# Kernel tuning notes

Measured on AMD Instinct MI355X. Metric: run time of the kernel, lower is better.

## Reference

```python
import jax, jax.numpy as jnp
import numpy as np

N_NODES = 50000   # n_nodes (adjacency is [N,N])
NNZ = 800000      # nonzeros per support (avg degree 16)
S = 3             # number of supports
D_IN = 512
D_OUT = 256


def setup_inputs() -> dict:
    key = jax.random.key(0)
    k0, k1, k2, k3, k4, k5 = jax.random.split(key, 6)
    x = jax.random.normal(k0, (N_NODES, D_IN), dtype=jnp.float32)
    # glorot-uniform per-support weights, stacked [S, D_IN, D_OUT]
    scale = float(np.sqrt(6.0 / (D_IN + D_OUT)))
    W = jax.random.uniform(k1, (S, D_IN, D_OUT), dtype=jnp.float32, minval=-scale, maxval=scale)
    rows = jax.random.randint(k2, (S, NNZ), 0, N_NODES, dtype=jnp.int32)
    cols = jax.random.randint(k3, (S, NNZ), 0, N_NODES, dtype=jnp.int32)
    vals = jax.random.uniform(k4, (S, NNZ), dtype=jnp.float32)
    # Conv1d(in=S, out=1, k=1, bias=False) == learned weighted sum over supports
    cw = jax.random.normal(k5, (S,), dtype=jnp.float32) * 0.5
    return {"x": x, "W": W, "rows": rows, "cols": cols, "vals": vals, "cw": cw}


def reference(x, W, rows, cols, vals, cw):
    # mod='output': out = relu( sum_i cw[i] * (A_i @ (x @ W_i)) )
    def spmm(r, c, v, pre):
        # A in COO: out[r] += v * pre[c]
        msgs = v[:, None] * pre[c]          # [NNZ, D_OUT] gather
        return jax.ops.segment_sum(msgs, r, num_segments=N_NODES)

    out = jnp.zeros((N_NODES, D_OUT), dtype=x.dtype)
    for i in range(S):                      # small fixed support count
        pre = x @ W[i]                      # dense GEMM [N, D_OUT]
        out = out + cw[i] * spmm(rows[i], cols[i], vals[i], pre)
    return jax.nn.relu(out)
```

## Files before the change

### kernel.cpp

```cpp
#include <hip/hip_runtime.h>
#include <stdint.h>

#define N_NODES 50000
#define N_PAD   50048
#define NNZ     800000
#define SUP     3
#define D_IN    512
#define D_OUT   256
#define TOT_E   (SUP * NNZ)
#define NBUCK   782
#define CAP     3680
#define CHUNK   3072
#define NBB     782
#define NB_WPREP 1536
#define NB_XPREP 12500
#define NB_GEMM  2346

typedef __attribute__((ext_vector_type(8))) short bf16x8;
typedef __attribute__((ext_vector_type(4))) float f32x4;
typedef __attribute__((address_space(3))) unsigned int lds_u32_t;
typedef const __attribute__((address_space(1))) unsigned int glb_u32_t;

static __device__ __forceinline__ unsigned short f2bf(float f) {
    unsigned int u = __float_as_uint(f);
    unsigned int r = (u + 0x7fffu + ((u >> 16) & 1u)) >> 16;
    return (unsigned short)r;
}
static __device__ __forceinline__ unsigned int pack_bf2(float lo, float hi) {
    unsigned int a = __float_as_uint(lo) + 0x8000u;
    unsigned int b = __float_as_uint(hi) + 0x8000u;
    return (a >> 16) | (b & 0xffff0000u);
}
static __device__ __forceinline__ float bf2f(unsigned short h) {
    return __uint_as_float(((unsigned int)h) << 16);
}
static __device__ __forceinline__ int2 ldnt_int2(const int2* p) {
    long long v = __builtin_nontemporal_load((const long long*)p);
    int2 r;
    r.x = (int)(v & 0xffffffffLL);
    r.y = (int)(v >> 32);
    return r;
}

__global__ __launch_bounds__(256) void prepbucket_kernel(const int* __restrict__ rows,
                                                         const int* __restrict__ cols,
                                                         const float* __restrict__ vals,
                                                         const float* __restrict__ cw,
                                                         int* __restrict__ bucket_cursor,
                                                         int2* __restrict__ buck,
                                                         const float* __restrict__ x,
                                                         unsigned int* __restrict__ xb,
                                                         const float* __restrict__ W,
                                                         unsigned short* __restrict__ Wt) {
    __shared__ double smem8[5536];
    char* smem = (char*)smem8;
    const int blk = blockIdx.x;
    const int tid = threadIdx.x;

    if (blk < NBB) {
        int2* stage = (int2*)smem;
        unsigned short* bucket_of = (unsigned short*)(smem + 24576);
        int* hist   = (int*)(smem + 30720);
        int* sc     = (int*)(smem + 33848);
        int* sstart = (int*)(smem + 34872);
        int* lcur   = (int*)(smem + 38000);
        int* gbase  = (int*)(smem + 41128);

        const int base_n = blk * CHUNK;
        const int count = min(CHUNK, TOT_E - base_n);
        float cw0 = cw[0], cw1 = cw[1], cw2 = cw[2];

        for (int i = tid; i < NBUCK; i += 256) hist[i] = 0;
        __syncthreads();
        for (int i = tid; i < count; i += 256)
            atomicAdd(&hist[rows[base_n + i] >> 6], 1);
        __syncthreads();
        const int lo = tid * 4;
        const int hi = min(lo + 4, NBUCK);
        int acc = 0;
        for (int i = lo; i < hi; ++i) acc += hist[i];
        sc[tid] = acc;
        __syncthreads();
        for (int off = 1; off < 256; off <<= 1) {
            int t = (tid >= off) ? sc[tid - off] : 0;
            __syncthreads();
            sc[tid] += t;
            __syncthreads();
        }
        int run = sc[tid] - acc;
        for (int i = lo; i < hi; ++i) {
            int h = hist[i];
            sstart[i] = run;
            lcur[i]   = run;
            run += h;
        }
        __syncthreads();
        for (int i = tid; i < NBUCK; i += 256)
            gbase[i] = atomicAdd(&bucket_cursor[i], hist[i]);
        __syncthreads();
        for (int i = tid; i < count; i += 256) {
            int n = base_n + i;
            int r = rows[n];
            int c = __builtin_nontemporal_load(&cols[n]);
            float v = __builtin_nontemporal_load(&vals[n]);
            int s = n / NNZ;
            float w = v * (s == 0 ? cw0 : (s == 1 ? cw1 : cw2));
            int b = r >> 6;
            int p = atomicAdd(&lcur[b], 1);
            stage[p] = make_int2(((r & 63) << 18) | (s * N_NODES + c), __float_as_int(w));
            bucket_of[p] = (unsigned short)b;
        }
        __syncthreads();
        for (int i = tid; i < count; i += 256) {
            int b = bucket_of[i];
            int local_off = i - sstart[b];
            buck[(size_t)b * CAP + gbase[b] + local_off] = stage[i];
        }
    } else if (blk < NBB + NB_XPREP) {
        int idx = (blk - NBB) * 256 + tid;
        const f32x4* src = (const f32x4*)(x) + idx * 2;
        f32x4 f0 = __builtin_nontemporal_load(src);
        f32x4 f1 = __builtin_nontemporal_load(src + 1);
        uint4 o;
        o.x = pack_bf2(f0.x, f0.y);
        o.y = pack_bf2(f0.z, f0.w);
        o.z = pack_bf2(f1.x, f1.y);
        o.w = pack_bf2(f1.z, f1.w);
        *((uint4*)xb + idx) = o;
    } else {
        int idx = (blk - NBB - NB_XPREP) * 256 + tid;
        int n = idx & (D_OUT - 1);
        int k = (idx >> 8) & (D_IN - 1);
        int s = idx >> 17;
        Wt[((size_t)s * D_OUT + n) * D_IN + k] = f2bf(W[idx]);
    }
}

__global__ __launch_bounds__(256) void sortgemm_kernel(const int2* __restrict__ buck,
                                                       const int* __restrict__ bucket_cursor,
                                                       int2* __restrict__ cv,
                                                       int* __restrict__ base,
                                                       int* __restrict__ cnt,
                                                       const unsigned short* __restrict__ xb,
                                                       const unsigned short* __restrict__ Wt,
                                                       unsigned short* __restrict__ pre) {
    __shared__ double smem8[4096];
    char* smem = (char*)smem8;
    const int blk = blockIdx.x;
    const int tid = threadIdx.x;

    if (blk < NBUCK) {
        int2* stage = (int2*)smem;
        int* hist   = (int*)(smem + 29440);
        int* sc     = (int*)(smem + 29696);
        int* sstart = (int*)(smem + 29952);
        int* cur    = (int*)(smem + 30208);

        const int b = blk;
        const int sz = bucket_cursor[b];
        const int2* src = buck + (size_t)b * CAP;

        if (tid < 64) hist[tid] = 0;
        __syncthreads();
        for (int i = tid; i < sz; i += 256)
            atomicAdd(&hist[((unsigned)src[i].x) >> 18], 1);
        __syncthreads();
        if (tid < 64) sc[tid] = hist[tid];
        __syncthreads();
        for (int off = 1; off < 64; off <<= 1) {
            int t = (tid >= off && tid < 64) ? sc[tid - off] : 0;
            __syncthreads();
            if (tid < 64) sc[tid] += t;
            __syncthreads();
        }
        if (tid < 64) {
            int st = sc[tid] - hist[tid];
            sstart[tid] = st;
            cur[tid] = st;
        }
        __syncthreads();
        for (int i = tid; i < sz; i += 256) {
            int2 e = src[i];
            int rl = ((unsigned)e.x) >> 18;
            int p = atomicAdd(&cur[rl], 1);
            stage[p] = make_int2(e.x & 0x3FFFF, e.y);
        }
        __syncthreads();
        size_t gb = (size_t)b * CAP;
        for (int i = tid; i < sz; i += 256) cv[gb + i] = stage[i];
        int r = b * 64 + tid;
        if (tid < 64 && r < N_NODES) {
            base[r] = (int)gb + sstart[tid];
            cnt[r]  = hist[tid];
        }
    } else {
        unsigned short* lds_a = (unsigned short*)smem;
        unsigned short* lds_b = (unsigned short*)(smem + 16384);
        const int gblk = blk - NBUCK;
        constexpr int SWQ = NB_GEMM / 8;
        constexpr int SWR = NB_GEMM % 8;
        const int xcd = gblk & 7, pos = gblk >> 3;
        const int my = (xcd < SWR ? xcd * (SWQ + 1)
                                  : SWR * (SWQ + 1) + (xcd - SWR) * SWQ) + pos;
        const int mt  = my / 6;
        const int rem = my % 6;
        const int m0 = mt * 128;
        const int n0 = (rem & 1) * 128;
        const int s  = rem >> 1;
        const unsigned short* wt = Wt + (size_t)s * D_OUT * D_IN;
        const int wave = tid >> 6;
        const int lane = tid & 63;
        const int quad = lane >> 4;
        const int lo   = lane & 15;
        const int wm = (wave & 1) * 64;
        const int wn = (wave >> 1) * 64;

        f32x4 acc[4][4] = {};

        for (int kb = 0; kb < D_IN; kb += 64) {
            __syncthreads();
            #pragma unroll
            for (int c = 0; c < 4; ++c) {
                int idx = c * 256 + tid;
                int row = idx >> 3;
                int kp  = idx & 7;
                const unsigned short* ga = xb + (size_t)(m0 + row) * D_IN + kb + kp * 8;
                __builtin_amdgcn_global_load_lds((glb_u32_t*)ga,
                                                 (lds_u32_t*)&lds_a[idx * 8], 16, 0, 0);
                const unsigned short* gb = wt + (size_t)(n0 + row) * D_IN + kb + kp * 8;
                __builtin_amdgcn_global_load_lds((glb_u32_t*)gb,
                                                 (lds_u32_t*)&lds_b[idx * 8], 16, 0, 0);
            }
            __syncthreads();

            #pragma unroll
            for (int t = 0; t < 2; ++t) {
                bf16x8 af[4], bfr[4];
                #pragma unroll
                for (int i = 0; i < 4; ++i)
                    af[i] = *(const bf16x8*)&lds_a[(wm + 16 * i + lo) * 64 + t * 32 + quad * 8];
                #pragma unroll
                for (int j = 0; j < 4; ++j)
                    bfr[j] = *(const bf16x8*)&lds_b[(wn + 16 * j + lo) * 64 + t * 32 + quad * 8];
                #pragma unroll
                for (int i = 0; i < 4; ++i)
                    #pragma unroll
                    for (int j = 0; j < 4; ++j)
                        acc[i][j] = __builtin_amdgcn_mfma_f32_16x16x32_bf16(af[i], bfr[j], acc[i][j], 0, 0, 0);
            }
        }

        #pragma unroll
        for (int i = 0; i < 4; ++i) {
            #pragma unroll
            for (int j = 0; j < 4; ++j) {
                int gn = n0 + wn + 16 * j + lo;
                #pragma unroll
                for (int r = 0; r < 4; ++r) {
                    int gm2 = m0 + wm + 16 * i + quad * 4 + r;
                    if (gm2 < N_NODES)
                        pre[((size_t)s * N_NODES + gm2) * D_OUT + gn] = f2bf(acc[i][j][r]);
                }
            }
        }
    }
}

__global__ __launch_bounds__(256) void spmm_kernel(const unsigned short* __restrict__ pre,
                                                   const int* __restrict__ base,
                                                   const int* __restrict__ cnt,
                                                   const int2* __restrict__ cv,
                                                   float* __restrict__ out) {
    int row  = blockIdx.x * 4 + (threadIdx.x >> 6);
    int lane = threadIdx.x & 63;
    int start = base[row];
    int end   = start + cnt[row];
    float a0 = 0.f, a1 = 0.f, a2 = 0.f, a3 = 0.f;
    int j = start;
    for (; j + 16 <= end; j += 16) {
        int2 e[16];
        #pragma unroll
        for (int q = 0; q < 16; ++q) e[q] = ldnt_int2(&cv[j + q]);
        ushort4 p[16];
        #pragma unroll
        for (int q = 0; q < 16; ++q)
            p[q] = *(const ushort4*)(pre + (size_t)e[q].x * D_OUT + lane * 4);
        #pragma unroll
        for (int q = 0; q < 16; ++q) {
            float w = __int_as_float(e[q].y);
            a0 += w * bf2f(p[q].x);
            a1 += w * bf2f(p[q].y);
            a2 += w * bf2f(p[q].z);
            a3 += w * bf2f(p[q].w);
        }
    }
    for (; j + 8 <= end; j += 8) {
        int2 e[8];
        #pragma unroll
        for (int q = 0; q < 8; ++q) e[q] = ldnt_int2(&cv[j + q]);
        ushort4 p[8];
        #pragma unroll
        for (int q = 0; q < 8; ++q)
            p[q] = *(const ushort4*)(pre + (size_t)e[q].x * D_OUT + lane * 4);
        #pragma unroll
        for (int q = 0; q < 8; ++q) {
            float w = __int_as_float(e[q].y);
            a0 += w * bf2f(p[q].x);
            a1 += w * bf2f(p[q].y);
            a2 += w * bf2f(p[q].z);
            a3 += w * bf2f(p[q].w);
        }
    }
    for (; j + 4 <= end; j += 4) {
        int2 e[4];
        #pragma unroll
        for (int q = 0; q < 4; ++q) e[q] = ldnt_int2(&cv[j + q]);
        ushort4 p[4];
        #pragma unroll
        for (int q = 0; q < 4; ++q)
            p[q] = *(const ushort4*)(pre + (size_t)e[q].x * D_OUT + lane * 4);
        #pragma unroll
        for (int q = 0; q < 4; ++q) {
            float w = __int_as_float(e[q].y);
            a0 += w * bf2f(p[q].x);
            a1 += w * bf2f(p[q].y);
            a2 += w * bf2f(p[q].z);
            a3 += w * bf2f(p[q].w);
        }
    }
    for (; j < end; ++j) {
        int2 e = ldnt_int2(&cv[j]);
        float w = __int_as_float(e.y);
        ushort4 p = *(const ushort4*)(pre + (size_t)e.x * D_OUT + lane * 4);
        a0 += w * bf2f(p.x);
        a1 += w * bf2f(p.y);
        a2 += w * bf2f(p.z);
        a3 += w * bf2f(p.w);
    }
    f32x4 o;
    o.x = fmaxf(a0, 0.f);
    o.y = fmaxf(a1, 0.f);
    o.z = fmaxf(a2, 0.f);
    o.w = fmaxf(a3, 0.f);
    __builtin_nontemporal_store(o, (f32x4*)(out + (size_t)row * D_OUT + lane * 4));
}

extern "C" void kernel_launch(void* const* d_in, const int* in_sizes, int n_in,
                              void* d_out, int out_size, void* d_ws, size_t ws_size,
                              hipStream_t stream) {
    const float* x    = (const float*)d_in[0];
    const float* W    = (const float*)d_in[1];
    const int*   rows = (const int*)d_in[2];
    const int*   cols = (const int*)d_in[3];
    const float* vals = (const float*)d_in[4];
    const float* cw   = (const float*)d_in[5];
    float* out = (float*)d_out;

    char* ws = (char*)d_ws;
    size_t off = 0;
    auto alloc = [&](size_t bytes) -> void* {
        void* p = ws + off;
        off += (bytes + 255) & ~(size_t)255;
        return p;
    };
    unsigned short* pre  = (unsigned short*)alloc((size_t)SUP * N_NODES * D_OUT * 2);
    unsigned short* xb   = (unsigned short*)alloc((size_t)N_PAD * D_IN * 2);
    unsigned short* Wt   = (unsigned short*)alloc((size_t)SUP * D_OUT * D_IN * 2);
    int* base            = (int*)alloc((size_t)N_NODES * 4);
    int* cnt             = (int*)alloc((size_t)N_NODES * 4);
    int* bucket_cursor   = (int*)alloc((size_t)NBUCK * 4);
    int2* cv             = (int2*)alloc((size_t)NBUCK * CAP * 8);
    int2* buck           = (int2*)d_out;

    hipMemsetAsync(bucket_cursor, 0, (size_t)NBUCK * 4, stream);

    prepbucket_kernel<<<NBB + NB_XPREP + NB_WPREP, 256, 0, stream>>>(
        rows, cols, vals, cw, bucket_cursor, buck, x, (unsigned int*)xb, W, Wt);
    sortgemm_kernel<<<NBUCK + NB_GEMM, 256, 0, stream>>>(
        buck, bucket_cursor, cv, base, cnt, xb, Wt, pre);
    spmm_kernel<<<N_NODES / 4, 256, 0, stream>>>(pre, base, cnt, cv, out);
}
```

Before: 477.7 us.

## Fuse x-to-bf16 conversion into GEMM A-tile load and pad bucket cursors

Removes the separate pass that converted x to a bf16 buffer. The GEMM now loads fp32 x directly through registers, packs it to bf16, and writes the A tile to LDS, clamping rows past the end of x. This saves one full write and re-read of x in bf16. In exchange, the GEMM reads twice as many bytes of x (fp32, re-read by each of the six N-tile and support blocks) and loses the direct global-to-LDS path for A. Bucket cursors are also spaced 16 ints apart to cut atomic contention and false sharing.

```diff
diff --git a/kernel.cpp b/kernel.cpp
--- a/kernel.cpp
+++ b/kernel.cpp
@@ -2,7 +2,6 @@
 #include <stdint.h>
 
 #define N_NODES 50000
-#define N_PAD   50048
 #define NNZ     800000
 #define SUP     3
 #define D_IN    512
@@ -12,8 +11,8 @@
 #define CAP     3680
 #define CHUNK   3072
 #define NBB     782
+#define CSTR    16
 #define NB_WPREP 1536
-#define NB_XPREP 12500
 #define NB_GEMM  2346
 
 typedef __attribute__((ext_vector_type(8))) short bf16x8;
@@ -48,8 +47,6 @@
                                                          const float* __restrict__ cw,
                                                          int* __restrict__ bucket_cursor,
                                                          int2* __restrict__ buck,
-                                                         const float* __restrict__ x,
-                                                         unsigned int* __restrict__ xb,
                                                          const float* __restrict__ W,
                                                          unsigned short* __restrict__ Wt) {
     __shared__ double smem8[5536];
@@ -96,7 +93,7 @@
         }
         __syncthreads();
         for (int i = tid; i < NBUCK; i += 256)
-            gbase[i] = atomicAdd(&bucket_cursor[i], hist[i]);
+            gbase[i] = atomicAdd(&bucket_cursor[i * CSTR], hist[i]);
         __syncthreads();
         for (int i = tid; i < count; i += 256) {
             int n = base_n + i;
@@ -116,19 +113,8 @@
             int local_off = i - sstart[b];
             buck[(size_t)b * CAP + gbase[b] + local_off] = stage[i];
         }
-    } else if (blk < NBB + NB_XPREP) {
+    } else {
         int idx = (blk - NBB) * 256 + tid;
-        const f32x4* src = (const f32x4*)(x) + idx * 2;
-        f32x4 f0 = __builtin_nontemporal_load(src);
-        f32x4 f1 = __builtin_nontemporal_load(src + 1);
-        uint4 o;
-        o.x = pack_bf2(f0.x, f0.y);
-        o.y = pack_bf2(f0.z, f0.w);
-        o.z = pack_bf2(f1.x, f1.y);
-        o.w = pack_bf2(f1.z, f1.w);
-        *((uint4*)xb + idx) = o;
-    } else {
-        int idx = (blk - NBB - NB_XPREP) * 256 + tid;
         int n = idx & (D_OUT - 1);
         int k = (idx >> 8) & (D_IN - 1);
         int s = idx >> 17;
@@ -141,7 +127,7 @@
                                                        int2* __restrict__ cv,
                                                        int* __restrict__ base,
                                                        int* __restrict__ cnt,
-                                                       const unsigned short* __restrict__ xb,
+                                                       const float* __restrict__ x,
                                                        const unsigned short* __restrict__ Wt,
                                                        unsigned short* __restrict__ pre) {
     __shared__ double smem8[4096];
@@ -157,7 +143,7 @@
         int* cur    = (int*)(smem + 30208);
 
         const int b = blk;
-        const int sz = bucket_cursor[b];
+        const int sz = bucket_cursor[b * CSTR];
         const int2* src = buck + (size_t)b * CAP;
 
         if (tid < 64) hist[tid] = 0;
@@ -215,21 +201,35 @@
         const int wm = (wave & 1) * 64;
         const int wn = (wave >> 1) * 64;
 
+        const int a_row = tid >> 3;
+        const int a_kp  = tid & 7;
+
         f32x4 acc[4][4] = {};
 
         for (int kb = 0; kb < D_IN; kb += 64) {
             __syncthreads();
+            f32x4 xa0[4], xa1[4];
+            #pragma unroll
+            for (int c = 0; c < 4; ++c) {
+                int row = c * 32 + a_row;
+                int grow = min(m0 + row, N_NODES - 1);
+                const f32x4* gp = (const f32x4*)(x + (size_t)grow * D_IN + kb + a_kp * 8);
+                xa0[c] = gp[0];
+                xa1[c] = gp[1];
+                int idx = c * 256 + tid;
+                const unsigned short* gb = wt + (size_t)(n0 + (idx >> 3)) * D_IN + kb + (idx & 7) * 8;
+                __builtin_amdgcn_global_load_lds((glb_u32_t*)gb,
+                                                 (lds_u32_t*)&lds_b[idx * 8], 16, 0, 0);
+            }
             #pragma unroll
             for (int c = 0; c < 4; ++c) {
                 int idx = c * 256 + tid;
-                int row = idx >> 3;
-                int kp  = idx & 7;
-                const unsigned short* ga = xb + (size_t)(m0 + row) * D_IN + kb + kp * 8;
-                __builtin_amdgcn_global_load_lds((glb_u32_t*)ga,
-                                                 (lds_u32_t*)&lds_a[idx * 8], 16, 0, 0);
-                const unsigned short* gb = wt + (size_t)(n0 + row) * D_IN + kb + kp * 8;
-                __builtin_amdgcn_global_load_lds((glb_u32_t*)gb,
-                                                 (lds_u32_t*)&lds_b[idx * 8], 16, 0, 0);
+                uint4 o;
+                o.x = pack_bf2(xa0[c].x, xa0[c].y);
+                o.y = pack_bf2(xa0[c].z, xa0[c].w);
+                o.z = pack_bf2(xa1[c].x, xa1[c].y);
+                o.w = pack_bf2(xa1[c].z, xa1[c].w);
+                *(uint4*)&lds_a[idx * 8] = o;
             }
             __syncthreads();
 
@@ -364,19 +364,18 @@
         return p;
     };
     unsigned short* pre  = (unsigned short*)alloc((size_t)SUP * N_NODES * D_OUT * 2);
-    unsigned short* xb   = (unsigned short*)alloc((size_t)N_PAD * D_IN * 2);
     unsigned short* Wt   = (unsigned short*)alloc((size_t)SUP * D_OUT * D_IN * 2);
     int* base            = (int*)alloc((size_t)N_NODES * 4);
     int* cnt             = (int*)alloc((size_t)N_NODES * 4);
-    int* bucket_cursor   = (int*)alloc((size_t)NBUCK * 4);
+    int* bucket_cursor   = (int*)alloc((size_t)NBUCK * CSTR * 4);
     int2* cv             = (int2*)alloc((size_t)NBUCK * CAP * 8);
     int2* buck           = (int2*)d_out;
 
-    hipMemsetAsync(bucket_cursor, 0, (size_t)NBUCK * 4, stream);
-
-    prepbucket_kernel<<<NBB + NB_XPREP + NB_WPREP, 256, 0, stream>>>(
-        rows, cols, vals, cw, bucket_cursor, buck, x, (unsigned int*)xb, W, Wt);
+    hipMemsetAsync(bucket_cursor, 0, (size_t)NBUCK * CSTR * 4, stream);
+
+    prepbucket_kernel<<<NBB + NB_WPREP, 256, 0, stream>>>(
+        rows, cols, vals, cw, bucket_cursor, buck, W, Wt);
     sortgemm_kernel<<<NBUCK + NB_GEMM, 256, 0, stream>>>(
-        buck, bucket_cursor, cv, base, cnt, xb, Wt, pre);
+        buck, bucket_cursor, cv, base, cnt, x, Wt, pre);
     spmm_kernel<<<N_NODES / 4, 256, 0, stream>>>(pre, base, cnt, cv, out);
 }
```

Measured after the change: 511.0 us. +7.0%, slower.
